# Kernel tuning notes

Hardware: AMD Instinct MI355X
Metric: run time of the kernel (lower is better)

Reference implementation:

```python
import jax, jax.numpy as jnp
import numpy as np

N = 50000
F = 128
E = 800000
HOP = 3
ALPHA = 0.2  # leaky relu slope


def setup_inputs() -> dict:
    key = jax.random.key(0)
    ks = jax.random.split(key, 6)
    x = jax.random.normal(ks[0], (N, F), dtype=jnp.float32)
    h0 = jax.random.normal(ks[1], (N, F), dtype=jnp.float32)
    edge_index = jax.random.randint(ks[2], (2, E), 0, N, dtype=jnp.int32)
    edge_weight = jax.random.uniform(ks[3], (E,), dtype=jnp.float32)
    # xavier-uniform-ish params
    lim_w = float(np.sqrt(6.0 / (F + F)))
    W_att = jax.random.uniform(ks[4], (F, F), dtype=jnp.float32, minval=-lim_w, maxval=lim_w)
    lim_a = 1.414 * float(np.sqrt(6.0 / (2 * F + 1)))
    a = jax.random.uniform(ks[5], (2 * F, 1), dtype=jnp.float32, minval=-lim_a, maxval=lim_a)
    temp = jnp.zeros((4,), dtype=jnp.float32)
    return {"x": x, "h0": h0, "edge_index": edge_index, "edge_weight": edge_weight,
            "W_att": W_att, "a": a, "temp": temp}


def _segment_softmax(e, rows, num_segments):
    m = jax.ops.segment_max(e, rows, num_segments=num_segments)
    m = jnp.where(jnp.isfinite(m), m, 0.0)  # guard empty rows
    ex = jnp.exp(e - m[rows])
    s = jax.ops.segment_sum(ex, rows, num_segments=num_segments)
    s = jnp.where(s > 0, s, 1.0)
    return ex / s[rows]


def reference(x, h0, edge_index, edge_weight, W_att, a, temp):
    rows, cols = edge_index[0], edge_index[1]
    # --- attention (edge-wise, never materializing dense NxN e) ---
    feat = x @ W_att                       # [N, F]
    f1 = (feat @ a[:F]).squeeze(-1)        # [N]
    f2 = (feat @ a[F:]).squeeze(-1)        # [N]
    e = f1[rows] + f2[cols]                # e[i,j] at edges
    e = jnp.where(e > 0, e, ALPHA * e)     # leaky relu
    att = _segment_softmax(e, rows, N)     # sparse row softmax values
    P = 0.5 * att
    # --- lifting bases ---
    coe = jax.nn.sigmoid(temp)
    rowsum = jax.ops.segment_sum(edge_weight * P, rows, num_segments=N)  # [N]
    update = x
    feat_prime = None
    for step in range(HOP):
        # sparse mm: U @ update
        update = jax.ops.segment_sum(att[:, None] * update[cols], rows, num_segments=N)
        feat_even = coe[0] * x + update
        feat_odd = update - feat_even * rowsum[:, None]
        feat_prime = feat_odd if step == 0 else coe[2] * feat_prime + (1.0 - coe[2]) * feat_odd
    return feat_prime
```

## Files before the change

kernel.cpp:

```cpp
#include <hip/hip_runtime.h>
#include <hip/hip_fp16.h>

#define NN 50000
#define FF 128
#define EE 800000
#define CAP 64
#define ALPHA 0.2f
#define ESHIFT 4.0f

__global__ void k_w(const float* __restrict__ W, const float* __restrict__ a,
                    float* __restrict__ w12) {
    int k = threadIdx.x;
    float s1 = 0.f, s2 = 0.f;
    const float* wr = W + k * FF;
    for (int j = 0; j < FF; ++j) {
        float w = wr[j];
        s1 += w * a[j];
        s2 += w * a[FF + j];
    }
    w12[k] = s1;
    w12[FF + k] = s2;
}

__global__ void k_f(const float* __restrict__ x, const float* __restrict__ w12,
                    float* __restrict__ f1, float* __restrict__ f2,
                    __half* __restrict__ xh) {
    int gid = blockIdx.x * blockDim.x + threadIdx.x;
    int node = gid >> 6;
    int lane = threadIdx.x & 63;
    if (node >= NN) return;
    float2 xv = ((const float2*)(x + (size_t)node * FF))[lane];
    ((__half2*)(xh + (size_t)node * FF))[lane] = __float22half2_rn(xv);
    float2 w1 = ((const float2*)w12)[lane];
    float2 w2 = ((const float2*)(w12 + FF))[lane];
    float s1 = xv.x * w1.x + xv.y * w1.y;
    float s2 = xv.x * w2.x + xv.y * w2.y;
#pragma unroll
    for (int o = 32; o > 0; o >>= 1) {
        s1 += __shfl_down(s1, o);
        s2 += __shfl_down(s2, o);
    }
    if (lane == 0) { f1[node] = s1; f2[node] = s2; }
}

__global__ void k_edge(const int* __restrict__ rows, const int* __restrict__ cols,
                       const float* __restrict__ ew, const float* __restrict__ f1,
                       const float* __restrict__ f2, int* __restrict__ fill,
                       int2* __restrict__ bucket) {
    int e = blockIdx.x * blockDim.x + threadIdx.x;
    if (e >= EE) return;
    int r = rows[e], c = cols[e];
    float v = f1[r] + f2[c];
    v = v > 0.f ? v : ALPHA * v;
    float ex = __expf(v - ESHIFT);
    union { int i; __half2 h; } p;
    p.h = __floats2half2_rn(ex, ew[e] * ex);
    int pos = atomicAdd(&fill[r], 1);
    if (pos < CAP) bucket[(size_t)r * CAP + pos] = make_int2(c, p.i);
}

__global__ void k_hop(const float* __restrict__ x, const __half* __restrict__ uin,
                      __half* __restrict__ uout, const int* __restrict__ fill,
                      const int2* __restrict__ bucket, const float* __restrict__ temp,
                      float* __restrict__ fp, int step) {
    int wave = threadIdx.x >> 6;
    int lane = threadIdx.x & 63;
    int r = __builtin_amdgcn_readfirstlane(blockIdx.x * 4 + wave);
    if (r >= NN) return;
    int d = fill[r];
    if (d > CAP) d = CAP;
    const int2* bk = bucket + (size_t)r * CAP;
    float ax = 0.f, ay = 0.f, se = 0.f, sw = 0.f;
    int j = 0;
    for (; j + 8 <= d; j += 8) {
        int2 b[8];
        __half2 h[8];
#pragma unroll
        for (int t = 0; t < 8; ++t) b[t] = bk[j + t];
#pragma unroll
        for (int t = 0; t < 8; ++t)
            h[t] = ((const __half2*)(uin + (size_t)b[t].x * FF))[lane];
#pragma unroll
        for (int t = 0; t < 8; ++t) {
            union { int i; __half2 h2; } p;
            p.i = b[t].y;
            float2 ee = __half22float2(p.h2);
            float2 u = __half22float2(h[t]);
            ax += ee.x * u.x;
            ay += ee.x * u.y;
            se += ee.x;
            sw += ee.y;
        }
    }
    for (; j < d; ++j) {
        int2 b = bk[j];
        __half2 hv = ((const __half2*)(uin + (size_t)b.x * FF))[lane];
        union { int i; __half2 h2; } p;
        p.i = b.y;
        float2 ee = __half22float2(p.h2);
        float2 u = __half22float2(hv);
        ax += ee.x * u.x;
        ay += ee.x * u.y;
        se += ee.x;
        sw += ee.y;
    }
    float inv = se > 0.f ? 1.f / se : 0.f;
    ax *= inv;
    ay *= inv;
    float rs = 0.5f * sw * inv;
    float coe0 = 1.f / (1.f + __expf(-temp[0]));
    float coe2 = 1.f / (1.f + __expf(-temp[2]));
    float2 xv = ((const float2*)(x + (size_t)r * FF))[lane];
    float evx = coe0 * xv.x + ax;
    float evy = coe0 * xv.y + ay;
    float ox = ax - evx * rs;
    float oy = ay - evy * rs;
    float2* fpr = (float2*)(fp + (size_t)r * FF);
    if (step == 0) {
        fpr[lane] = make_float2(ox, oy);
    } else {
        float2 p = fpr[lane];
        fpr[lane] = make_float2(coe2 * p.x + (1.f - coe2) * ox,
                                coe2 * p.y + (1.f - coe2) * oy);
    }
    if (step < 2) {
        ((__half2*)(uout + (size_t)r * FF))[lane] = __float22half2_rn(make_float2(ax, ay));
    }
}

extern "C" void kernel_launch(void* const* d_in, const int* in_sizes, int n_in,
                              void* d_out, int out_size, void* d_ws, size_t ws_size,
                              hipStream_t stream) {
    const float* x = (const float*)d_in[0];
    const int* eidx = (const int*)d_in[2];
    const int* rows = eidx;
    const int* cols = eidx + EE;
    const float* ew = (const float*)d_in[3];
    const float* W = (const float*)d_in[4];
    const float* a = (const float*)d_in[5];
    const float* temp = (const float*)d_in[6];
    float* out = (float*)d_out;

    float* ws = (float*)d_ws;
    int* fill = (int*)ws;
    float* f1 = ws + NN;
    float* f2 = ws + 2 * NN;
    float* w12 = ws + 3 * NN;
    int2* bucket = (int2*)(ws + 3 * NN + 256);
    __half* xh = (__half*)(bucket + (size_t)NN * CAP);
    __half* uh0 = xh + (size_t)NN * FF;
    __half* uh1 = xh;

    hipMemsetAsync(fill, 0, NN * sizeof(int), stream);

    k_w<<<1, 128, 0, stream>>>(W, a, w12);
    k_f<<<(NN + 3) / 4, 256, 0, stream>>>(x, w12, f1, f2, xh);
    k_edge<<<(EE + 255) / 256, 256, 0, stream>>>(rows, cols, ew, f1, f2, fill, bucket);
    k_hop<<<(NN + 3) / 4, 256, 0, stream>>>(x, xh, uh0, fill, bucket, temp, out, 0);
    k_hop<<<(NN + 3) / 4, 256, 0, stream>>>(x, uh0, uh1, fill, bucket, temp, out, 1);
    k_hop<<<(NN + 3) / 4, 256, 0, stream>>>(x, uh1, nullptr, fill, bucket, temp, out, 2);
}
```

Baseline: 295.2 us.

## Fold hop combination algebraically into fp16 accumulator; batch edges per thread; shrink bucket cap

The output recurrence is rewritten algebraically: hops 0 and 1 only accumulate weighted updates into an fp16 scratch buffer S, and the final hop applies the rowsum and x terms once, writing fp32 output a single time. This drops the fp32 output read/write in the early hops and the x loads there. The edge kernel now handles four strided edges per thread to overlap gathers and atomics, and the per-row bucket capacity drops from 64 to 48 to reduce bucket footprint. Risks are fp16 accumulation error in S and silently dropping edges for rows with degree above 48.

```diff
diff --git a/kernel.cpp b/kernel.cpp
--- a/kernel.cpp
+++ b/kernel.cpp
@@ -4,7 +4,7 @@
 #define NN 50000
 #define FF 128
 #define EE 800000
-#define CAP 64
+#define CAP 48
 #define ALPHA 0.2f
 #define ESHIFT 4.0f
 
@@ -47,22 +47,45 @@
                        const float* __restrict__ ew, const float* __restrict__ f1,
                        const float* __restrict__ f2, int* __restrict__ fill,
                        int2* __restrict__ bucket) {
-    int e = blockIdx.x * blockDim.x + threadIdx.x;
-    if (e >= EE) return;
-    int r = rows[e], c = cols[e];
-    float v = f1[r] + f2[c];
-    v = v > 0.f ? v : ALPHA * v;
-    float ex = __expf(v - ESHIFT);
-    union { int i; __half2 h; } p;
-    p.h = __floats2half2_rn(ex, ew[e] * ex);
-    int pos = atomicAdd(&fill[r], 1);
-    if (pos < CAP) bucket[(size_t)r * CAP + pos] = make_int2(c, p.i);
+    const int STR = EE / 4;
+    int t = blockIdx.x * blockDim.x + threadIdx.x;
+    if (t >= STR) return;
+    int r[4], c[4];
+    float w[4];
+#pragma unroll
+    for (int k = 0; k < 4; ++k) {
+        int e = t + k * STR;
+        r[k] = rows[e];
+        c[k] = cols[e];
+        w[k] = ew[e];
+    }
+    float f1v[4], f2v[4];
+#pragma unroll
+    for (int k = 0; k < 4; ++k) { f1v[k] = f1[r[k]]; f2v[k] = f2[c[k]]; }
+    int pay[4];
+#pragma unroll
+    for (int k = 0; k < 4; ++k) {
+        float v = f1v[k] + f2v[k];
+        v = v > 0.f ? v : ALPHA * v;
+        float ex = __expf(v - ESHIFT);
+        union { int i; __half2 h; } p;
+        p.h = __floats2half2_rn(ex, w[k] * ex);
+        pay[k] = p.i;
+    }
+    int pos[4];
+#pragma unroll
+    for (int k = 0; k < 4; ++k) pos[k] = atomicAdd(&fill[r[k]], 1);
+#pragma unroll
+    for (int k = 0; k < 4; ++k) {
+        if (pos[k] < CAP)
+            bucket[(size_t)r[k] * CAP + pos[k]] = make_int2(c[k], pay[k]);
+    }
 }
 
 __global__ void k_hop(const float* __restrict__ x, const __half* __restrict__ uin,
                       __half* __restrict__ uout, const int* __restrict__ fill,
                       const int2* __restrict__ bucket, const float* __restrict__ temp,
-                      float* __restrict__ fp, int step) {
+                      __half* __restrict__ S, float* __restrict__ out, int step) {
     int wave = threadIdx.x >> 6;
     int lane = threadIdx.x & 63;
     int r = __builtin_amdgcn_readfirstlane(blockIdx.x * 4 + wave);
@@ -107,24 +130,28 @@
     float inv = se > 0.f ? 1.f / se : 0.f;
     ax *= inv;
     ay *= inv;
-    float rs = 0.5f * sw * inv;
-    float coe0 = 1.f / (1.f + __expf(-temp[0]));
-    float coe2 = 1.f / (1.f + __expf(-temp[2]));
-    float2 xv = ((const float2*)(x + (size_t)r * FF))[lane];
-    float evx = coe0 * xv.x + ax;
-    float evy = coe0 * xv.y + ay;
-    float ox = ax - evx * rs;
-    float oy = ay - evy * rs;
-    float2* fpr = (float2*)(fp + (size_t)r * FF);
+    float c2 = 1.f / (1.f + __expf(-temp[2]));
+    __half2* Sr = (__half2*)(S + (size_t)r * FF);
     if (step == 0) {
-        fpr[lane] = make_float2(ox, oy);
+        ((__half2*)(uout + (size_t)r * FF))[lane] = __float22half2_rn(make_float2(ax, ay));
+        float w0 = c2 * c2;
+        Sr[lane] = __float22half2_rn(make_float2(w0 * ax, w0 * ay));
+    } else if (step == 1) {
+        ((__half2*)(uout + (size_t)r * FF))[lane] = __float22half2_rn(make_float2(ax, ay));
+        float w1 = c2 * (1.f - c2);
+        float2 sv = __half22float2(Sr[lane]);
+        Sr[lane] = __float22half2_rn(make_float2(sv.x + w1 * ax, sv.y + w1 * ay));
     } else {
-        float2 p = fpr[lane];
-        fpr[lane] = make_float2(coe2 * p.x + (1.f - coe2) * ox,
-                                coe2 * p.y + (1.f - coe2) * oy);
-    }
-    if (step < 2) {
-        ((__half2*)(uout + (size_t)r * FF))[lane] = __float22half2_rn(make_float2(ax, ay));
+        float rs = 0.5f * sw * inv;
+        float coe0 = 1.f / (1.f + __expf(-temp[0]));
+        float w2 = 1.f - c2;
+        float2 sv = __half22float2(Sr[lane]);
+        float2 xv = ((const float2*)(x + (size_t)r * FF))[lane];
+        float k1 = 1.f - rs;
+        float k2 = coe0 * rs;
+        ((float2*)(out + (size_t)r * FF))[lane] =
+            make_float2(k1 * (sv.x + w2 * ax) - k2 * xv.x,
+                        k1 * (sv.y + w2 * ay) - k2 * xv.y);
     }
 }
 
@@ -149,14 +176,15 @@
     int2* bucket = (int2*)(ws + 3 * NN + 256);
     __half* xh = (__half*)(bucket + (size_t)NN * CAP);
     __half* uh0 = xh + (size_t)NN * FF;
+    __half* Sb = uh0 + (size_t)NN * FF;
     __half* uh1 = xh;
 
     hipMemsetAsync(fill, 0, NN * sizeof(int), stream);
 
     k_w<<<1, 128, 0, stream>>>(W, a, w12);
     k_f<<<(NN + 3) / 4, 256, 0, stream>>>(x, w12, f1, f2, xh);
-    k_edge<<<(EE + 255) / 256, 256, 0, stream>>>(rows, cols, ew, f1, f2, fill, bucket);
-    k_hop<<<(NN + 3) / 4, 256, 0, stream>>>(x, xh, uh0, fill, bucket, temp, out, 0);
-    k_hop<<<(NN + 3) / 4, 256, 0, stream>>>(x, uh0, uh1, fill, bucket, temp, out, 1);
-    k_hop<<<(NN + 3) / 4, 256, 0, stream>>>(x, uh1, nullptr, fill, bucket, temp, out, 2);
+    k_edge<<<(EE / 4 + 255) / 256, 256, 0, stream>>>(rows, cols, ew, f1, f2, fill, bucket);
+    k_hop<<<(NN + 3) / 4, 256, 0, stream>>>(x, xh, uh0, fill, bucket, temp, Sb, out, 0);
+    k_hop<<<(NN + 3) / 4, 256, 0, stream>>>(x, uh0, uh1, fill, bucket, temp, Sb, out, 1);
+    k_hop<<<(NN + 3) / 4, 256, 0, stream>>>(x, uh1, nullptr, fill, bucket, temp, Sb, out, 2);
 }
```

New measurement: 283.9 us. -3.8%, faster.
